# Kernel tuning notes

Hardware: AMD Instinct MI355X
Metric: run time of the kernel (lower is better)

## Reference

```python
import jax, jax.numpy as jnp
import numpy as np

N_NODES = 100000
N_EDGES = 1600000
F_IN, HIDDEN, N_CLASS, K = 64, 64, 32, 3
DROPOUT_P = 0.5


def setup_inputs() -> dict:
    key = jax.random.key(0)
    ks = jax.random.split(key, 5)
    x = jax.random.normal(ks[0], (N_NODES, F_IN), dtype=jnp.float32)
    edge_index = jax.random.randint(ks[1], (2, N_EDGES), 0, N_NODES, dtype=jnp.int64)
    W1 = jax.random.normal(ks[2], (K, F_IN, HIDDEN), dtype=jnp.float32) * (1.0 / np.sqrt(F_IN))
    b1 = jnp.zeros((HIDDEN,), dtype=jnp.float32)
    W2 = jax.random.normal(ks[3], (K, HIDDEN, N_CLASS), dtype=jnp.float32) * (1.0 / np.sqrt(HIDDEN))
    b2 = jnp.zeros((N_CLASS,), dtype=jnp.float32)
    return {"x": x, "edge_index": edge_index, "W1": W1, "b1": b1, "W2": W2, "b2": b2}


def _cheb_norm(edge_index, n_nodes):
    # PyG ChebConv sym norm with lambda_max=2: L_hat = -D^{-1/2} A D^{-1/2}
    row, col = edge_index[0], edge_index[1]
    deg = jax.ops.segment_sum(jnp.ones_like(row, dtype=jnp.float32), row, num_segments=n_nodes)
    dinv = jnp.where(deg > 0, jax.lax.rsqrt(jnp.maximum(deg, 1.0)), 0.0)
    return -(dinv[row] * dinv[col])  # [E]


def _cheb_conv(x, row, col, norm, W, b):
    # Chebyshev recursion: Tx0=x, Tx1=L_hat x, Tx_k = 2 L_hat Tx_{k-1} - Tx_{k-2}
    def prop(h):
        return jax.ops.segment_sum(norm[:, None] * h[col], row, num_segments=h.shape[0])
    Tx0 = x
    out = Tx0 @ W[0]
    Tx1 = prop(Tx0)
    out = out + Tx1 @ W[1]
    for k in range(2, W.shape[0]):
        Tx2 = 2.0 * prop(Tx1) - Tx0
        out = out + Tx2 @ W[k]
        Tx0, Tx1 = Tx1, Tx2
    return out + b


def reference(x, edge_index, W1, b1, W2, b2):
    row, col = edge_index[0], edge_index[1]
    norm = _cheb_norm(edge_index, x.shape[0])
    h = jax.nn.relu(_cheb_conv(x, row, col, norm, W1, b1))
    # dropout (training=True) with fixed key, inverted scaling
    keep = jax.random.bernoulli(jax.random.key(42), 1.0 - DROPOUT_P, h.shape)
    h = jnp.where(keep, h / (1.0 - DROPOUT_P), 0.0)
    out = _cheb_conv(h, row, col, norm, W2, b2)
    return jax.nn.log_softmax(out, axis=-1)
```

## Files before the change

kernel.cpp:

```cpp
#include <hip/hip_runtime.h>


static constexpr int BLK = 256;
static constexpr int SCAN_CHUNK = 256;
static constexpr int ROWB = 256;
static constexpr int RB_SHIFT = 8;
static constexpr int BCAP = 6144;
static constexpr int CHUNK = 8192;

typedef _Float16 f16x8 __attribute__((ext_vector_type(8)));
typedef float f32x4 __attribute__((ext_vector_type(4)));

__device__ __forceinline__ unsigned rotl32(unsigned x, int r) {
    return (x << r) | (x >> (32 - r));
}

__device__ __forceinline__ unsigned tf_word(unsigned i) {
    const unsigned ks0 = 0u;
    const unsigned ks1 = 42u;
    const unsigned ks2 = 0u ^ 42u ^ 0x1BD11BDAu;
    unsigned x0 = 0u + ks0;
    unsigned x1 = i + ks1;
#define TF_RND(r) { x0 += x1; x1 = rotl32(x1, (r)); x1 ^= x0; }
    TF_RND(13) TF_RND(15) TF_RND(26) TF_RND(6)
    x0 += ks1; x1 += ks2 + 1u;
    TF_RND(17) TF_RND(29) TF_RND(16) TF_RND(24)
    x0 += ks2; x1 += ks0 + 2u;
    TF_RND(13) TF_RND(15) TF_RND(26) TF_RND(6)
    x0 += ks0; x1 += ks1 + 3u;
    TF_RND(17) TF_RND(29) TF_RND(16) TF_RND(24)
    x0 += ks1; x1 += ks2 + 4u;
    TF_RND(13) TF_RND(15) TF_RND(26) TF_RND(6)
    x0 += ks2; x1 += ks0 + 5u;
#undef TF_RND
    return x0 ^ x1;
}

__device__ __forceinline__ float lo16(unsigned u) {
    union { unsigned x; float f; } c; c.x = u << 16; return c.f;
}
__device__ __forceinline__ float hi16(unsigned u) {
    union { unsigned x; float f; } c; c.x = u & 0xFFFF0000u; return c.f;
}
__device__ __forceinline__ unsigned short f2b(float f) {
    union { float f; unsigned u; } c; c.f = f;
    unsigned r = (c.u + 0x7FFFu + ((c.u >> 16) & 1u)) >> 16;
    return (unsigned short)r;
}
__device__ __forceinline__ unsigned pack2(float a, float b) {
    return (unsigned)f2b(a) | ((unsigned)f2b(b) << 16);
}

__global__ void k_detect(const int* __restrict__ ei, int* __restrict__ flags) {
    __shared__ int cnt_nz;
    int t = threadIdx.x;
    if (t == 0) cnt_nz = 0;
    __syncthreads();
    if (ei[2 * t + 1] != 0) atomicAdd(&cnt_nz, 1);
    __syncthreads();
    if (t == 0) flags[0] = (cnt_nz == 0) ? 1 : 0;
}

__global__ void __launch_bounds__(256) k_bin(const int* __restrict__ ei, int E,
                                             const int* __restrict__ flags,
                                             int* __restrict__ bcnt,
                                             unsigned* __restrict__ bdata, int NB) {
    __shared__ unsigned sval[CHUNK];
    __shared__ unsigned short sbkt[CHUNK];
    __shared__ int h[512], ex[512], cur[512], basep[512];
    int t = threadIdx.x;
    int start = blockIdx.x * CHUNK;
    int lim = min(CHUNK, E - start);
    bool i64 = flags[0] != 0;
    h[t] = 0; h[t + 256] = 0;
    __syncthreads();
    unsigned vv[32];
    unsigned short bb_[32];
#pragma unroll
    for (int k = 0; k < 32; ++k) {
        int idx = k * 256 + t;
        int e = start + idx;
        if (idx < lim) {
            int r, c;
            if (i64) { r = ei[2 * e]; c = ei[2 * (E + e)]; }
            else     { r = ei[e];     c = ei[E + e]; }
            int b = r >> RB_SHIFT;
            vv[k] = ((unsigned)(r & (ROWB - 1)) << 17) | (unsigned)c;
            bb_[k] = (unsigned short)b;
            atomicAdd(&h[b], 1);
        } else {
            bb_[k] = 0xFFFF;
        }
    }
    __syncthreads();
    int i0 = t, i1 = t + 256;
    ex[i0] = h[i0]; ex[i1] = h[i1];
    __syncthreads();
    for (int off = 1; off < 512; off <<= 1) {
        int v0 = (i0 >= off) ? ex[i0 - off] : 0;
        int v1 = (i1 >= off) ? ex[i1 - off] : 0;
        __syncthreads();
        ex[i0] += v0; ex[i1] += v1;
        __syncthreads();
    }
    int e0 = ex[i0] - h[i0], e1 = ex[i1] - h[i1];
    __syncthreads();
    ex[i0] = e0; cur[i0] = e0;
    ex[i1] = e1; cur[i1] = e1;
    if (i0 < NB && h[i0] > 0) basep[i0] = atomicAdd(&bcnt[i0], h[i0]);
    if (i1 < NB && h[i1] > 0) basep[i1] = atomicAdd(&bcnt[i1], h[i1]);
    __syncthreads();
#pragma unroll
    for (int k = 0; k < 32; ++k) {
        if (bb_[k] != 0xFFFF) {
            int p = atomicAdd(&cur[bb_[k]], 1);
            sval[p] = vv[k];
            sbkt[p] = bb_[k];
        }
    }
    __syncthreads();
    for (int i = t; i < lim; i += 256) {
        int b = sbkt[i];
        int gpos = basep[b] + (i - ex[b]);
        if (gpos < BCAP) bdata[(size_t)b * BCAP + gpos] = sval[i];
    }
}

__global__ void __launch_bounds__(256) k_hist2(const unsigned* __restrict__ bdata,
                                               const int* __restrict__ bcnt,
                                               int N, int* __restrict__ deg) {
    __shared__ int h[ROWB];
    int t = threadIdx.x, b = blockIdx.x;
    h[t] = 0;
    __syncthreads();
    int cnt = min(bcnt[b], BCAP);
    for (int i = t; i < cnt; i += 256)
        atomicAdd(&h[bdata[(size_t)b * BCAP + i] >> 17], 1);
    __syncthreads();
    int r = b * ROWB + t;
    if (r < N) deg[r] = h[t];
}

__global__ void k_dinv(const int* __restrict__ deg, int N, float* __restrict__ dinv) {
    int v = blockIdx.x * blockDim.x + threadIdx.x;
    if (v < N) {
        int d = deg[v];
        dinv[v] = (d > 0) ? (1.0f / sqrtf((float)d)) : 0.0f;
    }
}

__global__ void k_scanA(const int* __restrict__ deg, int N, int* __restrict__ blk_sum) {
    __shared__ int lds[SCAN_CHUNK];
    int i = blockIdx.x * SCAN_CHUNK + threadIdx.x;
    int v = (i < N) ? deg[i] : 0;
    lds[threadIdx.x] = v;
    __syncthreads();
    for (int off = SCAN_CHUNK / 2; off > 0; off >>= 1) {
        if (threadIdx.x < off) lds[threadIdx.x] += lds[threadIdx.x + off];
        __syncthreads();
    }
    if (threadIdx.x == 0) blk_sum[blockIdx.x] = lds[0];
}

__global__ void k_scanB(int* __restrict__ blk_sum, int nb) {
    __shared__ int lds[1024];
    int t = threadIdx.x;
    int v = (t < nb) ? blk_sum[t] : 0;
    lds[t] = v;
    __syncthreads();
    for (int off = 1; off < 1024; off <<= 1) {
        int val = (t >= off) ? lds[t - off] : 0;
        __syncthreads();
        lds[t] += val;
        __syncthreads();
    }
    if (t < nb) blk_sum[t] = lds[t] - v;
}

__global__ void k_scanC(const int* __restrict__ deg, int N, int E,
                        const int* __restrict__ blk_sum, int* __restrict__ row_ptr) {
    __shared__ int lds[SCAN_CHUNK];
    int t = threadIdx.x;
    int i = blockIdx.x * SCAN_CHUNK + t;
    int v = (i < N) ? deg[i] : 0;
    lds[t] = v;
    __syncthreads();
    for (int off = 1; off < SCAN_CHUNK; off <<= 1) {
        int val = (t >= off) ? lds[t - off] : 0;
        __syncthreads();
        lds[t] += val;
        __syncthreads();
    }
    if (i < N) row_ptr[i] = blk_sum[blockIdx.x] + lds[t] - v;
    if (blockIdx.x == gridDim.x - 1 && t == SCAN_CHUNK - 1) row_ptr[N] = E;
}

__global__ void __launch_bounds__(256) k_place(const unsigned* __restrict__ bdata,
                                               const int* __restrict__ bcnt,
                                               const int* __restrict__ row_ptr,
                                               int N, int* __restrict__ sdst) {
    __shared__ int cur[ROWB];
    __shared__ int staged[BCAP];
    int t = threadIdx.x, b = blockIdx.x;
    int r0 = b * ROWB;
    int rbase = row_ptr[r0];
    int r = r0 + t;
    cur[t] = (r < N) ? (row_ptr[r] - rbase) : 0;
    __syncthreads();
    int cnt = min(bcnt[b], BCAP);
    for (int i = t; i < cnt; i += 256) {
        unsigned val = bdata[(size_t)b * BCAP + i];
        int p = atomicAdd(&cur[val >> 17], 1);
        staged[p] = (int)(val & 0x1FFFFu);
    }
    __syncthreads();
    for (int i = t; i < cnt; i += 256) sdst[rbase + i] = staged[i];
}

__global__ void k_wprep(const float* __restrict__ W1, const float* __restrict__ W2,
                        unsigned short* __restrict__ wt1,
                        unsigned short* __restrict__ wt2) {
    int idx = blockIdx.x * 256 + threadIdx.x;
    if (idx < 12288) {
        int c = idx >> 6, r6 = idx & 63;
        int slot = (r6 >> 3) ^ (c & 7);
        int k = slot * 8 + (r6 & 7);
        float v;
        if (c < 64)       v = W1[k * 64 + c] - W1[8192 + k * 64 + c];
        else if (c < 128) v = W1[4096 + k * 64 + (c - 64)];
        else              v = W1[8192 + k * 64 + (c - 128)];
        union { _Float16 h; unsigned short u; } cv; cv.h = (_Float16)v;
        wt1[idx] = cv.u;
    } else {
        int j = idx - 12288;
        int c = j >> 6, r6 = j & 63;
        int slot = (r6 >> 3) ^ (c & 7);
        int k = slot * 8 + (r6 & 7);
        float v;
        if (c < 32)      v = W2[k * 32 + c] - W2[4096 + k * 32 + c];
        else if (c < 64) v = W2[2048 + k * 32 + (c - 32)];
        else             v = W2[4096 + k * 32 + (c - 64)];
        union { _Float16 h; unsigned short u; } cv; cv.h = (_Float16)v;
        wt2[j] = cv.u;
    }
}

__global__ void __launch_bounds__(512) k_dense3(const float* __restrict__ x,
                                                const unsigned short* __restrict__ wt1,
                                                const float* __restrict__ b1,
                                                int N,
                                                unsigned short* __restrict__ B16,
                                                unsigned short* __restrict__ C16,
                                                float* __restrict__ D) {
    __shared__ unsigned short lds[20480] __attribute__((aligned(16)));
    __shared__ float sb[64];
    int t = threadIdx.x;
    int v0 = blockIdx.x * 128;
    {
        const uint4* src = (const uint4*)wt1;
        uint4* dst = (uint4*)&lds[8192];
        for (int i = t; i < 1536; i += 512) dst[i] = src[i];
    }
    if (t < 64) sb[t] = b1[t];
    {
        int row = t >> 2, c0 = (t & 3) << 4;
        int v = min(v0 + row, N - 1);
        const float* xp = x + (size_t)v * 64 + c0;
        float4 f0 = *(const float4*)xp;
        float4 f1 = *(const float4*)(xp + 4);
        float4 f2 = *(const float4*)(xp + 8);
        float4 f3 = *(const float4*)(xp + 12);
        int key = row & 7;
        int s0 = c0 >> 3;
        f16x8 h0, h1;
        h0[0] = (_Float16)f0.x; h0[1] = (_Float16)f0.y;
        h0[2] = (_Float16)f0.z; h0[3] = (_Float16)f0.w;
        h0[4] = (_Float16)f1.x; h0[5] = (_Float16)f1.y;
        h0[6] = (_Float16)f1.z; h0[7] = (_Float16)f1.w;
        h1[0] = (_Float16)f2.x; h1[1] = (_Float16)f2.y;
        h1[2] = (_Float16)f2.z; h1[3] = (_Float16)f2.w;
        h1[4] = (_Float16)f3.x; h1[5] = (_Float16)f3.y;
        h1[6] = (_Float16)f3.z; h1[7] = (_Float16)f3.w;
        *(f16x8*)&lds[row * 64 + ((s0 ^ key) << 3)] = h0;
        *(f16x8*)&lds[row * 64 + (((s0 + 1) ^ key) << 3)] = h1;
    }
    __syncthreads();

    int w = t >> 6, l = t & 63;
    int lr = l & 15, lk = l >> 4;
    int key = lr & 7;
    int arow = w * 16 + lr;
    f16x8 a0 = *(const f16x8*)&lds[arow * 64 + (((0 + lk) ^ key) << 3)];
    f16x8 a1 = *(const f16x8*)&lds[arow * 64 + (((4 + lk) ^ key) << 3)];
    f32x4 acc[12];
#pragma unroll
    for (int i = 0; i < 12; ++i) acc[i] = (f32x4){0.0f, 0.0f, 0.0f, 0.0f};
#pragma unroll
    for (int nt = 0; nt < 12; ++nt) {
        int bc = nt * 16 + lr;
        const unsigned short* wb = &lds[8192 + bc * 64];
        f16x8 b0 = *(const f16x8*)&wb[((0 + lk) ^ key) << 3];
        f16x8 b1v = *(const f16x8*)&wb[((4 + lk) ^ key) << 3];
        acc[nt] = __builtin_amdgcn_mfma_f32_16x16x32_f16(a0, b0, acc[nt], 0, 0, 0);
        acc[nt] = __builtin_amdgcn_mfma_f32_16x16x32_f16(a1, b1v, acc[nt], 0, 0, 0);
    }
#pragma unroll
    for (int nt = 0; nt < 4; ++nt) {
        int col = nt * 16 + lr;
        float bv = sb[col];
#pragma unroll
        for (int r = 0; r < 4; ++r) {
            int v = v0 + w * 16 + lk * 4 + r;
            if (v < N) D[(size_t)v * 64 + col] = acc[nt][r] + bv;
        }
    }
    __syncthreads();
#pragma unroll
    for (int nt = 4; nt < 12; ++nt) {
        int col = (nt - 4) * 16 + lr;
#pragma unroll
        for (int r = 0; r < 4; ++r) {
            int vloc = w * 16 + lk * 4 + r;
            lds[vloc * 128 + col] = f2b(acc[nt][r]);
        }
    }
    __syncthreads();
#pragma unroll
    for (int q = 0; q < 4; ++q) {
        int i = q * 512 + t;
        int row = i >> 4, ch = i & 15;
        int v = v0 + row;
        if (v < N) {
            uint4 val = *(const uint4*)&lds[i * 8];
            unsigned short* dst = (ch < 8)
                ? (B16 + (size_t)v * 64 + ch * 8)
                : (C16 + (size_t)v * 64 + (ch - 8) * 8);
            *(uint4*)dst = val;
        }
    }
}

__global__ void __launch_bounds__(512) k_dense3b(const unsigned short* __restrict__ wt2,
                                                 int N,
                                                 unsigned short* __restrict__ B16,
                                                 float* __restrict__ C) {
    __shared__ unsigned short lds[14336] __attribute__((aligned(16)));
    int t = threadIdx.x;
    int v0 = blockIdx.x * 128;
    {
        const uint4* src = (const uint4*)wt2;
        uint4* dst = (uint4*)&lds[8192];
        for (int i = t; i < 768; i += 512) dst[i] = src[i];
    }
    {
        int row = t >> 2, c0 = (t & 3) << 4;
        int v = min(v0 + row, N - 1);
        const float* xp = C + (size_t)v * 64 + c0;
        float4 f0 = *(const float4*)xp;
        float4 f1 = *(const float4*)(xp + 4);
        float4 f2 = *(const float4*)(xp + 8);
        float4 f3 = *(const float4*)(xp + 12);
        int key = row & 7;
        int s0 = c0 >> 3;
        f16x8 h0, h1;
        h0[0] = (_Float16)f0.x; h0[1] = (_Float16)f0.y;
        h0[2] = (_Float16)f0.z; h0[3] = (_Float16)f0.w;
        h0[4] = (_Float16)f1.x; h0[5] = (_Float16)f1.y;
        h0[6] = (_Float16)f1.z; h0[7] = (_Float16)f1.w;
        h1[0] = (_Float16)f2.x; h1[1] = (_Float16)f2.y;
        h1[2] = (_Float16)f2.z; h1[3] = (_Float16)f2.w;
        h1[4] = (_Float16)f3.x; h1[5] = (_Float16)f3.y;
        h1[6] = (_Float16)f3.z; h1[7] = (_Float16)f3.w;
        *(f16x8*)&lds[row * 64 + ((s0 ^ key) << 3)] = h0;
        *(f16x8*)&lds[row * 64 + (((s0 + 1) ^ key) << 3)] = h1;
    }
    __syncthreads();

    int w = t >> 6, l = t & 63;
    int lr = l & 15, lk = l >> 4;
    int key = lr & 7;
    int arow = w * 16 + lr;
    f16x8 a0 = *(const f16x8*)&lds[arow * 64 + (((0 + lk) ^ key) << 3)];
    f16x8 a1 = *(const f16x8*)&lds[arow * 64 + (((4 + lk) ^ key) << 3)];
    f32x4 acc[6];
#pragma unroll
    for (int i = 0; i < 6; ++i) acc[i] = (f32x4){0.0f, 0.0f, 0.0f, 0.0f};
#pragma unroll
    for (int nt = 0; nt < 6; ++nt) {
        int bc = nt * 16 + lr;
        const unsigned short* wb = &lds[8192 + bc * 64];
        f16x8 b0 = *(const f16x8*)&wb[((0 + lk) ^ key) << 3];
        f16x8 b1v = *(const f16x8*)&wb[((4 + lk) ^ key) << 3];
        acc[nt] = __builtin_amdgcn_mfma_f32_16x16x32_f16(a0, b0, acc[nt], 0, 0, 0);
        acc[nt] = __builtin_amdgcn_mfma_f32_16x16x32_f16(a1, b1v, acc[nt], 0, 0, 0);
    }
#pragma unroll
    for (int nt = 0; nt < 4; ++nt) {
        int col = nt * 16 + lr;
#pragma unroll
        for (int r = 0; r < 4; ++r) {
            int v = v0 + w * 16 + lk * 4 + r;
            if (v < N) C[(size_t)v * 64 + col] = acc[nt][r];
        }
    }
    __syncthreads();
#pragma unroll
    for (int nt = 4; nt < 6; ++nt) {
        int col = (nt - 4) * 16 + lr;
#pragma unroll
        for (int r = 0; r < 4; ++r) {
            int vloc = w * 16 + lk * 4 + r;
            lds[vloc * 32 + col] = f2b(acc[nt][r]);
        }
    }
    __syncthreads();
    {
        int i = t;
        int row = i >> 2, ch = i & 3;
        int v = v0 + row;
        if (v < N) {
            uint4 val = *(const uint4*)&lds[i * 8];
            *(uint4*)(B16 + (size_t)v * 32 + ch * 8) = val;
        }
    }
}

template <int NG>
__device__ __forceinline__ void gatherB(const unsigned short* __restrict__ src,
                                        int pitch,
                                        const float* __restrict__ dinv,
                                        const int* __restrict__ sdst,
                                        int beg, int end, int grp, int fl,
                                        float a[8]) {
#pragma unroll
    for (int q = 0; q < 8; ++q) a[q] = 0.0f;
    int e = beg + grp;
    for (; e + NG < end; e += 2 * NG) {
        int c0 = sdst[e];
        int c1 = sdst[e + NG];
        float w0 = dinv[c0], w1 = dinv[c1];
        uint4 r0 = *(const uint4*)(src + (size_t)c0 * pitch + 8 * fl);
        uint4 r1 = *(const uint4*)(src + (size_t)c1 * pitch + 8 * fl);
        a[0] = fmaf(w0, lo16(r0.x), a[0]); a[1] = fmaf(w0, hi16(r0.x), a[1]);
        a[2] = fmaf(w0, lo16(r0.y), a[2]); a[3] = fmaf(w0, hi16(r0.y), a[3]);
        a[4] = fmaf(w0, lo16(r0.z), a[4]); a[5] = fmaf(w0, hi16(r0.z), a[5]);
        a[6] = fmaf(w0, lo16(r0.w), a[6]); a[7] = fmaf(w0, hi16(r0.w), a[7]);
        a[0] = fmaf(w1, lo16(r1.x), a[0]); a[1] = fmaf(w1, hi16(r1.x), a[1]);
        a[2] = fmaf(w1, lo16(r1.y), a[2]); a[3] = fmaf(w1, hi16(r1.y), a[3]);
        a[4] = fmaf(w1, lo16(r1.z), a[4]); a[5] = fmaf(w1, hi16(r1.z), a[5]);
        a[6] = fmaf(w1, lo16(r1.w), a[6]); a[7] = fmaf(w1, hi16(r1.w), a[7]);
    }
    if (e < end) {
        int c = sdst[e];
        float w = dinv[c];
        uint4 r = *(const uint4*)(src + (size_t)c * pitch + 8 * fl);
        a[0] = fmaf(w, lo16(r.x), a[0]); a[1] = fmaf(w, hi16(r.x), a[1]);
        a[2] = fmaf(w, lo16(r.y), a[2]); a[3] = fmaf(w, hi16(r.y), a[3]);
        a[4] = fmaf(w, lo16(r.z), a[4]); a[5] = fmaf(w, hi16(r.z), a[5]);
        a[6] = fmaf(w, lo16(r.w), a[6]); a[7] = fmaf(w, hi16(r.w), a[7]);
    }
#pragma unroll
    for (int m = 64 / NG; m < 64; m <<= 1) {
#pragma unroll
        for (int q = 0; q < 8; ++q) a[q] += __shfl_xor(a[q], m);
    }
}

__global__ void __launch_bounds__(BLK) k_gath1(const unsigned short* __restrict__ C16,
                                               unsigned short* __restrict__ B16,
                                               const float* __restrict__ dinv,
                                               const int* __restrict__ row_ptr,
                                               const int* __restrict__ sdst,
                                               int N) {
    int v = blockIdx.x * 4 + (threadIdx.x >> 6);
    if (v >= N) return;
    int lane = threadIdx.x & 63;
    int grp = lane >> 3, fl = lane & 7;
    float a[8];
    gatherB<8>(C16, 64, dinv, sdst, row_ptr[v], row_ptr[v + 1], grp, fl, a);
    if (grp == 0) {
        float dv = -2.0f * dinv[v];
        unsigned short* p = B16 + (size_t)v * 64 + 8 * fl;
        uint4 b = *(const uint4*)p;
        float q0 = fmaf(dv, a[0], lo16(b.x)), q1 = fmaf(dv, a[1], hi16(b.x));
        float q2 = fmaf(dv, a[2], lo16(b.y)), q3 = fmaf(dv, a[3], hi16(b.y));
        float q4 = fmaf(dv, a[4], lo16(b.z)), q5 = fmaf(dv, a[5], hi16(b.z));
        float q6 = fmaf(dv, a[6], lo16(b.w)), q7 = fmaf(dv, a[7], hi16(b.w));
        uint4 o;
        o.x = pack2(q0, q1); o.y = pack2(q2, q3);
        o.z = pack2(q4, q5); o.w = pack2(q6, q7);
        *(uint4*)p = o;
    }
}

__global__ void __launch_bounds__(BLK) k_gath2(const float* __restrict__ D,
                                               const unsigned short* __restrict__ B16,
                                               float* __restrict__ C,
                                               const float* __restrict__ dinv,
                                               const int* __restrict__ row_ptr,
                                               const int* __restrict__ sdst,
                                               int N) {
    int v = blockIdx.x * 4 + (threadIdx.x >> 6);
    if (v >= N) return;
    int lane = threadIdx.x & 63;
    int grp = lane >> 3, fl = lane & 7;
    float a[8];
    gatherB<8>(B16, 64, dinv, sdst, row_ptr[v], row_ptr[v + 1], grp, fl, a);
    unsigned w = tf_word((unsigned)v * 64u + (unsigned)lane);
    unsigned ww[8];
#pragma unroll
    for (int k = 0; k < 8; ++k) ww[k] = __shfl(w, 8 * fl + k);
    if (grp == 0) {
        float dv = -dinv[v];
        const float* dp = D + (size_t)v * 64 + 8 * fl;
        float4 dA = *(const float4*)dp;
        float4 dB = *(const float4*)(dp + 4);
        float o[8];
        o[0] = fmaxf(fmaf(dv, a[0], dA.x), 0.0f);
        o[1] = fmaxf(fmaf(dv, a[1], dA.y), 0.0f);
        o[2] = fmaxf(fmaf(dv, a[2], dA.z), 0.0f);
        o[3] = fmaxf(fmaf(dv, a[3], dA.w), 0.0f);
        o[4] = fmaxf(fmaf(dv, a[4], dB.x), 0.0f);
        o[5] = fmaxf(fmaf(dv, a[5], dB.y), 0.0f);
        o[6] = fmaxf(fmaf(dv, a[6], dB.z), 0.0f);
        o[7] = fmaxf(fmaf(dv, a[7], dB.w), 0.0f);
#pragma unroll
        for (int k = 0; k < 8; ++k)
            o[k] = (ww[k] & 0x80000000u) ? 0.0f : o[k] * 2.0f;
        float* cp = C + (size_t)v * 64 + 8 * fl;
        *(float4*)cp = make_float4(o[0], o[1], o[2], o[3]);
        *(float4*)(cp + 4) = make_float4(o[4], o[5], o[6], o[7]);
    }
}

__global__ void __launch_bounds__(BLK) k_gath3(const unsigned short* __restrict__ B16,
                                               const float* __restrict__ C,
                                               unsigned short* __restrict__ R16,
                                               const float* __restrict__ dinv,
                                               const int* __restrict__ row_ptr,
                                               const int* __restrict__ sdst,
                                               int N) {
    int v = blockIdx.x * 4 + (threadIdx.x >> 6);
    if (v >= N) return;
    int lane = threadIdx.x & 63;
    int grp = lane >> 2, fl = lane & 3;
    float a[8];
    gatherB<16>(B16, 32, dinv, sdst, row_ptr[v], row_ptr[v + 1], grp, fl, a);
    if (grp == 0) {
        float dv = -2.0f * dinv[v];
        const float* dp = C + (size_t)v * 64 + 32 + 8 * fl;
        float4 dA = *(const float4*)dp;
        float4 dB = *(const float4*)(dp + 4);
        uint4 o;
        o.x = pack2(fmaf(dv, a[0], dA.x), fmaf(dv, a[1], dA.y));
        o.y = pack2(fmaf(dv, a[2], dA.z), fmaf(dv, a[3], dA.w));
        o.z = pack2(fmaf(dv, a[4], dB.x), fmaf(dv, a[5], dB.y));
        o.w = pack2(fmaf(dv, a[6], dB.z), fmaf(dv, a[7], dB.w));
        *(uint4*)(R16 + (size_t)v * 32 + 8 * fl) = o;
    }
}

__global__ void __launch_bounds__(BLK) k_gath4(const unsigned short* __restrict__ R16,
                                               const float* __restrict__ C,
                                               const float* __restrict__ dinv,
                                               const int* __restrict__ row_ptr,
                                               const int* __restrict__ sdst,
                                               const float* __restrict__ b2,
                                               int N, float* __restrict__ out) {
    int v = blockIdx.x * 4 + (threadIdx.x >> 6);
    if (v >= N) return;
    int lane = threadIdx.x & 63;
    int grp = lane >> 2, fl = lane & 3;
    float a[8];
    gatherB<16>(R16, 32, dinv, sdst, row_ptr[v], row_ptr[v + 1], grp, fl, a);
    float dv = -dinv[v];
    const float* dp = C + (size_t)v * 64 + 8 * fl;
    float4 dA = *(const float4*)dp;
    float4 dB = *(const float4*)(dp + 4);
    const float* bp = b2 + 8 * fl;
    float4 bA = *(const float4*)bp;
    float4 bB = *(const float4*)(bp + 4);
    float o[8];
    o[0] = fmaf(dv, a[0], dA.x + bA.x);
    o[1] = fmaf(dv, a[1], dA.y + bA.y);
    o[2] = fmaf(dv, a[2], dA.z + bA.z);
    o[3] = fmaf(dv, a[3], dA.w + bA.w);
    o[4] = fmaf(dv, a[4], dB.x + bB.x);
    o[5] = fmaf(dv, a[5], dB.y + bB.y);
    o[6] = fmaf(dv, a[6], dB.z + bB.z);
    o[7] = fmaf(dv, a[7], dB.w + bB.w);
    float m = o[0];
#pragma unroll
    for (int k = 1; k < 8; ++k) m = fmaxf(m, o[k]);
    m = fmaxf(m, __shfl_xor(m, 1));
    m = fmaxf(m, __shfl_xor(m, 2));
    float s = 0.0f;
#pragma unroll
    for (int k = 0; k < 8; ++k) s += expf(o[k] - m);
    s += __shfl_xor(s, 1);
    s += __shfl_xor(s, 2);
    float lse = m + logf(s);
    if (grp == 0) {
        float* op = out + (size_t)v * 32 + 8 * fl;
        *(float4*)op = make_float4(o[0] - lse, o[1] - lse, o[2] - lse, o[3] - lse);
        *(float4*)(op + 4) = make_float4(o[4] - lse, o[5] - lse, o[6] - lse, o[7] - lse);
    }
}

extern "C" void kernel_launch(void* const* d_in, const int* in_sizes, int n_in,
                              void* d_out, int out_size, void* d_ws, size_t ws_size,
                              hipStream_t stream) {
    const float* x  = (const float*)d_in[0];
    const int* ei   = (const int*)d_in[1];
    const float* W1 = (const float*)d_in[2];
    const float* b1 = (const float*)d_in[3];
    const float* W2 = (const float*)d_in[4];
    const float* b2 = (const float*)d_in[5];
    float* out = (float*)d_out;

    const int N = in_sizes[0] / 64;
    const int E = in_sizes[1] / 2;
    const int NB = (N + ROWB - 1) >> RB_SHIFT;

    char* ws = (char*)d_ws;
    size_t off = 0;
    auto alloc = [&](size_t bytes) -> void* {
        void* p = ws + off;
        off = (off + bytes + 511) & ~(size_t)511;
        return p;
    };
    int*      flags   = (int*)alloc(16);
    int*      deg     = (int*)alloc((size_t)N * 4);
    float*    dinv    = (float*)alloc((size_t)N * 4);
    int*      row_ptr = (int*)alloc(((size_t)N + 1) * 4);
    int*      blk_sum = (int*)alloc(4096);
    int*      bcnt    = (int*)alloc((size_t)NB * 4);
    size_t dbytes = (size_t)N * 64 * 4;
    size_t bdbytes = (size_t)NB * BCAP * 4;
    unsigned* bdata = (unsigned*)alloc(dbytes > bdbytes ? dbytes : bdbytes);
    float*    D     = (float*)bdata;
    int*      sdst  = (int*)alloc((size_t)E * 4);
    float*    C     = (float*)alloc((size_t)N * 64 * 4);
    unsigned short* B16 = (unsigned short*)alloc((size_t)N * 64 * 2);
    unsigned short* C16 = (unsigned short*)alloc((size_t)N * 64 * 2);
    unsigned short* R16 = C16;
    unsigned short* wt1 = (unsigned short*)alloc(12288 * 2);
    unsigned short* wt2 = (unsigned short*)alloc(6144 * 2);

    hipMemsetAsync(bcnt, 0, (size_t)NB * 4, stream);

    const int gN = (N + BLK - 1) / BLK;
    const int gW4 = (N + 3) / 4;
    const int gDM = (N + 127) / 128;
    const int nb = (N + SCAN_CHUNK - 1) / SCAN_CHUNK;
    const int gBin = (E + CHUNK - 1) / CHUNK;

    k_wprep<<<72, 256, 0, stream>>>(W1, W2, wt1, wt2);
    k_detect<<<1, 256, 0, stream>>>(ei, flags);
    k_bin<<<gBin, 256, 0, stream>>>(ei, E, flags, bcnt, bdata, NB);
    k_hist2<<<NB, 256, 0, stream>>>(bdata, bcnt, N, deg);
    k_dinv<<<gN, BLK, 0, stream>>>(deg, N, dinv);
    k_scanA<<<nb, SCAN_CHUNK, 0, stream>>>(deg, N, blk_sum);
    k_scanB<<<1, 1024, 0, stream>>>(blk_sum, nb);
    k_scanC<<<nb, SCAN_CHUNK, 0, stream>>>(deg, N, E, blk_sum, row_ptr);
    k_place<<<NB, 256, 0, stream>>>(bdata, bcnt, row_ptr, N, sdst);

    k_dense3<<<gDM, 512, 0, stream>>>(x, wt1, b1, N, B16, C16, D);
    k_gath1<<<gW4, BLK, 0, stream>>>(C16, B16, dinv, row_ptr, sdst, N);
    k_gath2<<<gW4, BLK, 0, stream>>>(D, B16, C, dinv, row_ptr, sdst, N);

    k_dense3b<<<gDM, 512, 0, stream>>>(wt2, N, B16, C);
    k_gath3<<<gW4, BLK, 0, stream>>>(B16, C, R16, dinv, row_ptr, sdst, N);
    k_gath4<<<gW4, BLK, 0, stream>>>(R16, C, dinv, row_ptr, sdst, b2, N, out);
}
```

Measured before the change: 339.3 us.

## Pre-scale gathered features by dinv and use half-wave per node gathers

Folds the source-side dinv factor into the producer kernels (dense GEMM epilogues and gather outputs), so each edge gather does a plain add instead of an extra dinv[c] load plus FMA. Gather kernels now assign 32 lanes per node instead of 64, which packs more nodes per block. Also fuses the dinv computation into the histogram kernel, splits the second-layer fp32 buffer into two compact 32-column arrays, and uses fast exp/log. The risks are slightly different fp16 rounding from pre-scaling and lower per-node memory parallelism on high-degree rows.

Result: faster. 282.7 us (-16.7%).

```diff
diff --git a/kernel.cpp b/kernel.cpp
--- a/kernel.cpp
+++ b/kernel.cpp
@@ -128,7 +128,8 @@
 
 __global__ void __launch_bounds__(256) k_hist2(const unsigned* __restrict__ bdata,
                                                const int* __restrict__ bcnt,
-                                               int N, int* __restrict__ deg) {
+                                               int N, int* __restrict__ deg,
+                                               float* __restrict__ dinv) {
     __shared__ int h[ROWB];
     int t = threadIdx.x, b = blockIdx.x;
     h[t] = 0;
@@ -138,14 +139,10 @@
         atomicAdd(&h[bdata[(size_t)b * BCAP + i] >> 17], 1);
     __syncthreads();
     int r = b * ROWB + t;
-    if (r < N) deg[r] = h[t];
-}
-
-__global__ void k_dinv(const int* __restrict__ deg, int N, float* __restrict__ dinv) {
-    int v = blockIdx.x * blockDim.x + threadIdx.x;
-    if (v < N) {
-        int d = deg[v];
-        dinv[v] = (d > 0) ? (1.0f / sqrtf((float)d)) : 0.0f;
+    if (r < N) {
+        int d = h[t];
+        deg[r] = d;
+        dinv[r] = (d > 0) ? rsqrtf((float)d) : 0.0f;
     }
 }
 
@@ -248,6 +245,7 @@
 __global__ void __launch_bounds__(512) k_dense3(const float* __restrict__ x,
                                                 const unsigned short* __restrict__ wt1,
                                                 const float* __restrict__ b1,
+                                                const float* __restrict__ dinv,
                                                 int N,
                                                 unsigned short* __restrict__ B16,
                                                 unsigned short* __restrict__ C16,
@@ -304,6 +302,8 @@
         acc[nt] = __builtin_amdgcn_mfma_f32_16x16x32_f16(a0, b0, acc[nt], 0, 0, 0);
         acc[nt] = __builtin_amdgcn_mfma_f32_16x16x32_f16(a1, b1v, acc[nt], 0, 0, 0);
     }
+    float4 dv4 = *(const float4*)&dinv[v0 + w * 16 + lk * 4];
+    float dsc[4] = {dv4.x, dv4.y, dv4.z, dv4.w};
 #pragma unroll
     for (int nt = 0; nt < 4; ++nt) {
         int col = nt * 16 + lr;
@@ -316,12 +316,21 @@
     }
     __syncthreads();
 #pragma unroll
-    for (int nt = 4; nt < 12; ++nt) {
+    for (int nt = 4; nt < 8; ++nt) {
         int col = (nt - 4) * 16 + lr;
 #pragma unroll
         for (int r = 0; r < 4; ++r) {
             int vloc = w * 16 + lk * 4 + r;
             lds[vloc * 128 + col] = f2b(acc[nt][r]);
+        }
+    }
+#pragma unroll
+    for (int nt = 8; nt < 12; ++nt) {
+        int col = (nt - 4) * 16 + lr;
+#pragma unroll
+        for (int r = 0; r < 4; ++r) {
+            int vloc = w * 16 + lk * 4 + r;
+            lds[vloc * 128 + col] = f2b(acc[nt][r] * dsc[r]);
         }
     }
     __syncthreads();
@@ -341,9 +350,12 @@
 }
 
 __global__ void __launch_bounds__(512) k_dense3b(const unsigned short* __restrict__ wt2,
+                                                 const float* __restrict__ dinv,
                                                  int N,
                                                  unsigned short* __restrict__ B16,
-                                                 float* __restrict__ C) {
+                                                 const float* __restrict__ C,
+                                                 float* __restrict__ P0,
+                                                 float* __restrict__ P1) {
     __shared__ unsigned short lds[14336] __attribute__((aligned(16)));
     int t = threadIdx.x;
     int v0 = blockIdx.x * 128;
@@ -394,13 +406,16 @@
         acc[nt] = __builtin_amdgcn_mfma_f32_16x16x32_f16(a0, b0, acc[nt], 0, 0, 0);
         acc[nt] = __builtin_amdgcn_mfma_f32_16x16x32_f16(a1, b1v, acc[nt], 0, 0, 0);
     }
+    float4 dv4 = *(const float4*)&dinv[v0 + w * 16 + lk * 4];
+    float dsc[4] = {dv4.x, dv4.y, dv4.z, dv4.w};
 #pragma unroll
     for (int nt = 0; nt < 4; ++nt) {
-        int col = nt * 16 + lr;
+        int col = (nt & 1) * 16 + lr;
+        float* dst = (nt < 2) ? P0 : P1;
 #pragma unroll
         for (int r = 0; r < 4; ++r) {
             int v = v0 + w * 16 + lk * 4 + r;
-            if (v < N) C[(size_t)v * 64 + col] = acc[nt][r];
+            if (v < N) dst[(size_t)v * 32 + col] = acc[nt][r];
         }
     }
     __syncthreads();
@@ -410,7 +425,7 @@
 #pragma unroll
         for (int r = 0; r < 4; ++r) {
             int vloc = w * 16 + lk * 4 + r;
-            lds[vloc * 32 + col] = f2b(acc[nt][r]);
+            lds[vloc * 32 + col] = f2b(acc[nt][r] * dsc[r]);
         }
     }
     __syncthreads();
@@ -425,42 +440,39 @@
     }
 }
 
-template <int NG>
-__device__ __forceinline__ void gatherB(const unsigned short* __restrict__ src,
-                                        int pitch,
-                                        const float* __restrict__ dinv,
+template <int PITCH>
+__device__ __forceinline__ void gatherH(const unsigned short* __restrict__ src,
                                         const int* __restrict__ sdst,
                                         int beg, int end, int grp, int fl,
                                         float a[8]) {
+    constexpr int NG = 32 / (PITCH / 8);
 #pragma unroll
     for (int q = 0; q < 8; ++q) a[q] = 0.0f;
     int e = beg + grp;
     for (; e + NG < end; e += 2 * NG) {
         int c0 = sdst[e];
         int c1 = sdst[e + NG];
-        float w0 = dinv[c0], w1 = dinv[c1];
-        uint4 r0 = *(const uint4*)(src + (size_t)c0 * pitch + 8 * fl);
-        uint4 r1 = *(const uint4*)(src + (size_t)c1 * pitch + 8 * fl);
-        a[0] = fmaf(w0, lo16(r0.x), a[0]); a[1] = fmaf(w0, hi16(r0.x), a[1]);
-        a[2] = fmaf(w0, lo16(r0.y), a[2]); a[3] = fmaf(w0, hi16(r0.y), a[3]);
-        a[4] = fmaf(w0, lo16(r0.z), a[4]); a[5] = fmaf(w0, hi16(r0.z), a[5]);
-        a[6] = fmaf(w0, lo16(r0.w), a[6]); a[7] = fmaf(w0, hi16(r0.w), a[7]);
-        a[0] = fmaf(w1, lo16(r1.x), a[0]); a[1] = fmaf(w1, hi16(r1.x), a[1]);
-        a[2] = fmaf(w1, lo16(r1.y), a[2]); a[3] = fmaf(w1, hi16(r1.y), a[3]);
-        a[4] = fmaf(w1, lo16(r1.z), a[4]); a[5] = fmaf(w1, hi16(r1.z), a[5]);
-        a[6] = fmaf(w1, lo16(r1.w), a[6]); a[7] = fmaf(w1, hi16(r1.w), a[7]);
+        uint4 r0 = *(const uint4*)(src + (size_t)c0 * PITCH + 8 * fl);
+        uint4 r1 = *(const uint4*)(src + (size_t)c1 * PITCH + 8 * fl);
+        a[0] += lo16(r0.x); a[1] += hi16(r0.x);
+        a[2] += lo16(r0.y); a[3] += hi16(r0.y);
+        a[4] += lo16(r0.z); a[5] += hi16(r0.z);
+        a[6] += lo16(r0.w); a[7] += hi16(r0.w);
+        a[0] += lo16(r1.x); a[1] += hi16(r1.x);
+        a[2] += lo16(r1.y); a[3] += hi16(r1.y);
+        a[4] += lo16(r1.z); a[5] += hi16(r1.z);
+        a[6] += lo16(r1.w); a[7] += hi16(r1.w);
     }
     if (e < end) {
         int c = sdst[e];
-        float w = dinv[c];
-        uint4 r = *(const uint4*)(src + (size_t)c * pitch + 8 * fl);
-        a[0] = fmaf(w, lo16(r.x), a[0]); a[1] = fmaf(w, hi16(r.x), a[1]);
-        a[2] = fmaf(w, lo16(r.y), a[2]); a[3] = fmaf(w, hi16(r.y), a[3]);
-        a[4] = fmaf(w, lo16(r.z), a[4]); a[5] = fmaf(w, hi16(r.z), a[5]);
-        a[6] = fmaf(w, lo16(r.w), a[6]); a[7] = fmaf(w, hi16(r.w), a[7]);
-    }
-#pragma unroll
-    for (int m = 64 / NG; m < 64; m <<= 1) {
+        uint4 r = *(const uint4*)(src + (size_t)c * PITCH + 8 * fl);
+        a[0] += lo16(r.x); a[1] += hi16(r.x);
+        a[2] += lo16(r.y); a[3] += hi16(r.y);
+        a[4] += lo16(r.z); a[5] += hi16(r.z);
+        a[6] += lo16(r.w); a[7] += hi16(r.w);
+    }
+#pragma unroll
+    for (int m = PITCH / 8; m < 32; m <<= 1) {
 #pragma unroll
         for (int q = 0; q < 8; ++q) a[q] += __shfl_xor(a[q], m);
     }
@@ -472,20 +484,21 @@
                                                const int* __restrict__ row_ptr,
                                                const int* __restrict__ sdst,
                                                int N) {
-    int v = blockIdx.x * 4 + (threadIdx.x >> 6);
+    int v = blockIdx.x * 8 + (threadIdx.x >> 5);
     if (v >= N) return;
-    int lane = threadIdx.x & 63;
-    int grp = lane >> 3, fl = lane & 7;
+    int hl = threadIdx.x & 31;
+    int grp = hl >> 3, fl = hl & 7;
     float a[8];
-    gatherB<8>(C16, 64, dinv, sdst, row_ptr[v], row_ptr[v + 1], grp, fl, a);
+    gatherH<64>(C16, sdst, row_ptr[v], row_ptr[v + 1], grp, fl, a);
     if (grp == 0) {
-        float dv = -2.0f * dinv[v];
+        float di = dinv[v];
+        float dv = -2.0f * di;
         unsigned short* p = B16 + (size_t)v * 64 + 8 * fl;
         uint4 b = *(const uint4*)p;
-        float q0 = fmaf(dv, a[0], lo16(b.x)), q1 = fmaf(dv, a[1], hi16(b.x));
-        float q2 = fmaf(dv, a[2], lo16(b.y)), q3 = fmaf(dv, a[3], hi16(b.y));
-        float q4 = fmaf(dv, a[4], lo16(b.z)), q5 = fmaf(dv, a[5], hi16(b.z));
-        float q6 = fmaf(dv, a[6], lo16(b.w)), q7 = fmaf(dv, a[7], hi16(b.w));
+        float q0 = di * fmaf(dv, a[0], lo16(b.x)), q1 = di * fmaf(dv, a[1], hi16(b.x));
+        float q2 = di * fmaf(dv, a[2], lo16(b.y)), q3 = di * fmaf(dv, a[3], hi16(b.y));
+        float q4 = di * fmaf(dv, a[4], lo16(b.z)), q5 = di * fmaf(dv, a[5], hi16(b.z));
+        float q6 = di * fmaf(dv, a[6], lo16(b.w)), q7 = di * fmaf(dv, a[7], hi16(b.w));
         uint4 o;
         o.x = pack2(q0, q1); o.y = pack2(q2, q3);
         o.z = pack2(q4, q5); o.w = pack2(q6, q7);
@@ -500,16 +513,19 @@
                                                const int* __restrict__ row_ptr,
                                                const int* __restrict__ sdst,
                                                int N) {
-    int v = blockIdx.x * 4 + (threadIdx.x >> 6);
+    int v = blockIdx.x * 8 + (threadIdx.x >> 5);
     if (v >= N) return;
     int lane = threadIdx.x & 63;
-    int grp = lane >> 3, fl = lane & 7;
+    int hl = lane & 31;
+    int grp = hl >> 3, fl = hl & 7;
     float a[8];
-    gatherB<8>(B16, 64, dinv, sdst, row_ptr[v], row_ptr[v + 1], grp, fl, a);
-    unsigned w = tf_word((unsigned)v * 64u + (unsigned)lane);
+    gatherH<64>(B16, sdst, row_ptr[v], row_ptr[v + 1], grp, fl, a);
+    unsigned wA = tf_word((unsigned)v * 64u + 2u * (unsigned)hl);
+    unsigned wB = tf_word((unsigned)v * 64u + 2u * (unsigned)hl + 1u);
+    int base = (lane & 32) + 4 * fl;
     unsigned ww[8];
 #pragma unroll
-    for (int k = 0; k < 8; ++k) ww[k] = __shfl(w, 8 * fl + k);
+    for (int k = 0; k < 8; ++k) ww[k] = __shfl((k & 1) ? wB : wA, base + (k >> 1));
     if (grp == 0) {
         float dv = -dinv[v];
         const float* dp = D + (size_t)v * 64 + 8 * fl;
@@ -534,47 +550,48 @@
 }
 
 __global__ void __launch_bounds__(BLK) k_gath3(const unsigned short* __restrict__ B16,
-                                               const float* __restrict__ C,
+                                               const float* __restrict__ P1,
                                                unsigned short* __restrict__ R16,
                                                const float* __restrict__ dinv,
                                                const int* __restrict__ row_ptr,
                                                const int* __restrict__ sdst,
                                                int N) {
-    int v = blockIdx.x * 4 + (threadIdx.x >> 6);
+    int v = blockIdx.x * 8 + (threadIdx.x >> 5);
     if (v >= N) return;
-    int lane = threadIdx.x & 63;
-    int grp = lane >> 2, fl = lane & 3;
+    int hl = threadIdx.x & 31;
+    int grp = hl >> 2, fl = hl & 3;
     float a[8];
-    gatherB<16>(B16, 32, dinv, sdst, row_ptr[v], row_ptr[v + 1], grp, fl, a);
+    gatherH<32>(B16, sdst, row_ptr[v], row_ptr[v + 1], grp, fl, a);
     if (grp == 0) {
-        float dv = -2.0f * dinv[v];
-        const float* dp = C + (size_t)v * 64 + 32 + 8 * fl;
+        float di = dinv[v];
+        float dv = -2.0f * di;
+        const float* dp = P1 + (size_t)v * 32 + 8 * fl;
         float4 dA = *(const float4*)dp;
         float4 dB = *(const float4*)(dp + 4);
         uint4 o;
-        o.x = pack2(fmaf(dv, a[0], dA.x), fmaf(dv, a[1], dA.y));
-        o.y = pack2(fmaf(dv, a[2], dA.z), fmaf(dv, a[3], dA.w));
-        o.z = pack2(fmaf(dv, a[4], dB.x), fmaf(dv, a[5], dB.y));
-        o.w = pack2(fmaf(dv, a[6], dB.z), fmaf(dv, a[7], dB.w));
+        o.x = pack2(di * fmaf(dv, a[0], dA.x), di * fmaf(dv, a[1], dA.y));
+        o.y = pack2(di * fmaf(dv, a[2], dA.z), di * fmaf(dv, a[3], dA.w));
+        o.z = pack2(di * fmaf(dv, a[4], dB.x), di * fmaf(dv, a[5], dB.y));
+        o.w = pack2(di * fmaf(dv, a[6], dB.z), di * fmaf(dv, a[7], dB.w));
         *(uint4*)(R16 + (size_t)v * 32 + 8 * fl) = o;
     }
 }
 
 __global__ void __launch_bounds__(BLK) k_gath4(const unsigned short* __restrict__ R16,
-                                               const float* __restrict__ C,
+                                               const float* __restrict__ P0,
                                                const float* __restrict__ dinv,
                                                const int* __restrict__ row_ptr,
                                                const int* __restrict__ sdst,
                                                const float* __restrict__ b2,
                                                int N, float* __restrict__ out) {
-    int v = blockIdx.x * 4 + (threadIdx.x >> 6);
+    int v = blockIdx.x * 8 + (threadIdx.x >> 5);
     if (v >= N) return;
-    int lane = threadIdx.x & 63;
-    int grp = lane >> 2, fl = lane & 3;
+    int hl = threadIdx.x & 31;
+    int grp = hl >> 2, fl = hl & 3;
     float a[8];
-    gatherB<16>(R16, 32, dinv, sdst, row_ptr[v], row_ptr[v + 1], grp, fl, a);
+    gatherH<32>(R16, sdst, row_ptr[v], row_ptr[v + 1], grp, fl, a);
     float dv = -dinv[v];
-    const float* dp = C + (size_t)v * 64 + 8 * fl;
+    const float* dp = P0 + (size_t)v * 32 + 8 * fl;
     float4 dA = *(const float4*)dp;
     float4 dB = *(const float4*)(dp + 4);
     const float* bp = b2 + 8 * fl;
@@ -596,10 +613,10 @@
     m = fmaxf(m, __shfl_xor(m, 2));
     float s = 0.0f;
 #pragma unroll
-    for (int k = 0; k < 8; ++k) s += expf(o[k] - m);
+    for (int k = 0; k < 8; ++k) s += __expf(o[k] - m);
     s += __shfl_xor(s, 1);
     s += __shfl_xor(s, 2);
-    float lse = m + logf(s);
+    float lse = m + __logf(s);
     if (grp == 0) {
         float* op = out + (size_t)v * 32 + 8 * fl;
         *(float4*)op = make_float4(o[0] - lse, o[1] - lse, o[2] - lse, o[3] - lse);
@@ -639,6 +656,8 @@
     size_t bdbytes = (size_t)NB * BCAP * 4;
     unsigned* bdata = (unsigned*)alloc(dbytes > bdbytes ? dbytes : bdbytes);
     float*    D     = (float*)bdata;
+    float*    P0    = (float*)bdata;
+    float*    P1    = P0 + (size_t)N * 32;
     int*      sdst  = (int*)alloc((size_t)E * 4);
     float*    C     = (float*)alloc((size_t)N * 64 * 4);
     unsigned short* B16 = (unsigned short*)alloc((size_t)N * 64 * 2);
@@ -649,8 +668,7 @@
 
     hipMemsetAsync(bcnt, 0, (size_t)NB * 4, stream);
 
-    const int gN = (N + BLK - 1) / BLK;
-    const int gW4 = (N + 3) / 4;
+    const int gW8 = (N + 7) / 8;
     const int gDM = (N + 127) / 128;
     const int nb = (N + SCAN_CHUNK - 1) / SCAN_CHUNK;
     const int gBin = (E + CHUNK - 1) / CHUNK;
@@ -658,18 +676,17 @@
     k_wprep<<<72, 256, 0, stream>>>(W1, W2, wt1, wt2);
     k_detect<<<1, 256, 0, stream>>>(ei, flags);
     k_bin<<<gBin, 256, 0, stream>>>(ei, E, flags, bcnt, bdata, NB);
-    k_hist2<<<NB, 256, 0, stream>>>(bdata, bcnt, N, deg);
-    k_dinv<<<gN, BLK, 0, stream>>>(deg, N, dinv);
+    k_hist2<<<NB, 256, 0, stream>>>(bdata, bcnt, N, deg, dinv);
     k_scanA<<<nb, SCAN_CHUNK, 0, stream>>>(deg, N, blk_sum);
     k_scanB<<<1, 1024, 0, stream>>>(blk_sum, nb);
     k_scanC<<<nb, SCAN_CHUNK, 0, stream>>>(deg, N, E, blk_sum, row_ptr);
     k_place<<<NB, 256, 0, stream>>>(bdata, bcnt, row_ptr, N, sdst);
 
-    k_dense3<<<gDM, 512, 0, stream>>>(x, wt1, b1, N, B16, C16, D);
-    k_gath1<<<gW4, BLK, 0, stream>>>(C16, B16, dinv, row_ptr, sdst, N);
-    k_gath2<<<gW4, BLK, 0, stream>>>(D, B16, C, dinv, row_ptr, sdst, N);
-
-    k_dense3b<<<gDM, 512, 0, stream>>>(wt2, N, B16, C);
-    k_gath3<<<gW4, BLK, 0, stream>>>(B16, C, R16, dinv, row_ptr, sdst, N);
-    k_gath4<<<gW4, BLK, 0, stream>>>(R16, C, dinv, row_ptr, sdst, b2, N, out);
-}
+    k_dense3<<<gDM, 512, 0, stream>>>(x, wt1, b1, dinv, N, B16, C16, D);
+    k_gath1<<<gW8, BLK, 0, stream>>>(C16, B16, dinv, row_ptr, sdst, N);
+    k_gath2<<<gW8, BLK, 0, stream>>>(D, B16, C, dinv, row_ptr, sdst, N);
+
+    k_dense3b<<<gDM, 512, 0, stream>>>(wt2, dinv, N, B16, C, P0, P1);
+    k_gath3<<<gW8, BLK, 0, stream>>>(B16, P1, R16, dinv, row_ptr, sdst, N);
+    k_gath4<<<gW8, BLK, 0, stream>>>(R16, P0, dinv, row_ptr, sdst, b2, N, out);
+}
```
